# Kernel tuning notes

Measured on AMD Instinct MI355X. Metric: run time of the kernel, lower is better.

## Reference

```python
import jax, jax.numpy as jnp
import numpy as np

B, T, D, N = 4, 1024, 1024, 16
H = D // N
SCALE = H ** -0.5
NEG_INF = float('-inf')


def setup_inputs() -> dict:
    key = jax.random.key(0)
    ks = jax.random.split(key, 6)
    x = jax.random.normal(ks[0], (B, T, D), dtype=jnp.float32)
    key_padding_mask = jax.random.uniform(ks[1], (B, T)) < 0.1  # True = padded key
    # xavier-ish scaling for weights
    proj_weight = jax.random.normal(ks[2], (3 * D, D), dtype=jnp.float32) * (2.0 / (4 * D)) ** 0.5
    proj_bias = jnp.zeros((3 * D,), dtype=jnp.float32)
    sign_w = jax.random.normal(ks[3], (2 * D, D), dtype=jnp.float32) * (2.0 / (3 * D)) ** 0.5
    sign_b = jnp.zeros((2 * D,), dtype=jnp.float32)
    out_w = jax.random.normal(ks[4], (D, D), dtype=jnp.float32) * (1.0 / D) ** 0.5
    out_b = jnp.zeros((D,), dtype=jnp.float32)
    return {"x": x, "key_padding_mask": key_padding_mask,
            "proj_weight": proj_weight, "proj_bias": proj_bias,
            "sign_w": sign_w, "sign_b": sign_b,
            "out_w": out_w, "out_b": out_b}


def _heads(t):
    # [B, S, D] -> [B, N, S, H]
    return t.reshape(t.shape[0], t.shape[1], N, H).transpose(0, 2, 1, 3)


def reference(x, key_padding_mask, proj_weight, proj_bias, sign_w, sign_b, out_w, out_b):
    # self-attention path: fused in-projection, chunk order is (k, v, q)
    kvq = x @ proj_weight.T + proj_bias            # [B, T, 3D]
    k, v, q = jnp.split(kvq, 3, axis=-1)
    # sign projections (sign_q and sign_k both enabled): chunk into (sq, sk)
    sqk = x @ sign_w.T + sign_b                    # [B, T, 2D]
    sq, sk = jnp.split(sqk, 2, axis=-1)

    q, k, v = _heads(q), _heads(k), _heads(v)      # [B, N, T, H]
    sq = jax.nn.relu(_heads(sq))                   # q_activation = relu
    sk = jax.nn.relu(_heads(sk))                   # k_activation = relu

    attn_weight = jnp.einsum('bnth,bnsh->bnts', q, k) * SCALE   # [B, N, T, T]
    sign_weight = jnp.tanh(jnp.einsum('bnth,bnsh->bnts', sq, sk))

    kp = key_padding_mask[:, None, None, :]        # [B, 1, 1, T]
    attn_weight = jnp.where(kp, NEG_INF, attn_weight)
    sign_weight = jnp.where(attn_weight == NEG_INF, 0.0, sign_weight)

    ctx = jnp.einsum('bnts,bnsh->bnth', sign_weight, v)         # [B, N, T, H]
    ctx = ctx.transpose(0, 2, 1, 3).reshape(x.shape[0], x.shape[1], D)
    out = ctx @ out_w.T + out_b
    return out, sign_weight
```

## Files before the change

kernel.cpp:

```cpp
#include <hip/hip_runtime.h>

#define B_ 4
#define T_ 1024
#define D_ 1024
#define N_ 16
#define H_ 64

typedef __attribute__((ext_vector_type(8))) short bf16x8;
typedef __attribute__((ext_vector_type(4))) float f32x4;

static __device__ __forceinline__ unsigned short f2bf(float f) {
  unsigned u = __float_as_uint(f);
  u += 0x7fff + ((u >> 16) & 1);
  return (unsigned short)(u >> 16);
}

static __device__ __forceinline__ unsigned pk2(float a, float b) {
  return (unsigned)f2bf(a) | ((unsigned)f2bf(b) << 16);
}

static __device__ __forceinline__ float fast_tanh(float x) {
  float e = __expf(2.0f * x);
  return 1.0f - 2.0f / (e + 1.0f);
}

__global__ __launch_bounds__(256) void prep_kernel(
    const float* __restrict__ x, const float* __restrict__ sign_w,
    const float* __restrict__ proj_w_v, const float* __restrict__ out_w,
    const unsigned char* __restrict__ raw,
    unsigned short* __restrict__ xb, unsigned short* __restrict__ swb,
    unsigned short* __restrict__ pwb, unsigned short* __restrict__ owb,
    unsigned long long* __restrict__ mask64) {
  if (blockIdx.x == 0) {
    __shared__ int s_flag;
    if (threadIdx.x == 0) s_flag = 0;
    __syncthreads();
    int any = 0;
    for (int i = threadIdx.x; i < 4096; i += 256)
      if (i & 3) any |= (int)raw[i];
    if (any) atomicOr(&s_flag, 1);
    __syncthreads();
    int byte_mode = s_flag;
    const int* iraw = (const int*)raw;
    int w = threadIdx.x >> 6, l = threadIdx.x & 63;
    for (int k = 0; k < 16; ++k) {
      int pair = w * 16 + k;
      int idx = pair * 64 + l;
      int v = byte_mode ? (int)raw[idx] : iraw[idx];
      unsigned long long bal = __ballot(v != 0);
      if (l == 0) mask64[pair] = bal;
    }
  }
  const int n0 = 1048576, n1 = 524288, n2 = 262144;
  const int total = n0 + n1 + n2 + 262144;
  for (int i = blockIdx.x * 256 + threadIdx.x; i < total;
       i += gridDim.x * 256) {
    const float* src;
    unsigned short* dst;
    int off;
    if (i < n0) { src = x; dst = xb; off = i; }
    else if (i < n0 + n1) { src = sign_w; dst = swb; off = i - n0; }
    else if (i < n0 + n1 + n2) { src = proj_w_v; dst = pwb; off = i - n0 - n1; }
    else { src = out_w; dst = owb; off = i - n0 - n1 - n2; }
    float4 v = ((const float4*)src)[off];
    uint2 pk;
    pk.x = pk2(v.x, v.y);
    pk.y = pk2(v.z, v.w);
    ((uint2*)dst)[off] = pk;
  }
}

__global__ __launch_bounds__(256, 3) void gemm_mfma_kernel(
    const unsigned short* __restrict__ A, const unsigned short* __restrict__ W,
    const float* __restrict__ bias, void* __restrict__ Cv,
    int M, int N, int K, int relu, int out_mode) {
  __shared__ __align__(16) unsigned short As[128 * 64];
  __shared__ __align__(16) unsigned short Ws[128 * 64];
  int tid = threadIdx.x;
  int l = tid & 63, w = tid >> 6;
  int l15 = l & 15, l4 = l >> 4;
  int wr = w >> 1, wc = w & 1;
  size_t bm = (size_t)blockIdx.x * 128, bn = (size_t)blockIdx.y * 128;

  f32x4 acc[4][4];
#pragma unroll
  for (int m = 0; m < 4; ++m)
#pragma unroll
    for (int n = 0; n < 4; ++n) acc[m][n] = (f32x4){0.f, 0.f, 0.f, 0.f};

  for (int k0 = 0; k0 < K; k0 += 64) {
    __syncthreads();
#pragma unroll
    for (int i = 0; i < 4; ++i) {
      int seg = i * 256 + tid;
      int row = seg >> 3, cb = (seg & 7) << 4;
      unsigned short* lA = As + (size_t)(i * 256 + w * 64) * 8;
      unsigned short* lW = Ws + (size_t)(i * 256 + w * 64) * 8;
      __builtin_amdgcn_global_load_lds(
          (const __attribute__((address_space(1))) void*)
              ((const char*)(A + (bm + row) * K + k0) + cb),
          (__attribute__((address_space(3))) void*)lA, 16, 0, 0);
      __builtin_amdgcn_global_load_lds(
          (const __attribute__((address_space(1))) void*)
              ((const char*)(W + (bn + row) * K + k0) + cb),
          (__attribute__((address_space(3))) void*)lW, 16, 0, 0);
    }
    __syncthreads();

#pragma unroll
    for (int ks = 0; ks < 2; ++ks) {
      bf16x8 af[4], bf[4];
#pragma unroll
      for (int m = 0; m < 4; ++m)
        af[m] = *(const bf16x8*)(As + (wr * 64 + m * 16 + l15) * 64 +
                                 ks * 32 + l4 * 8);
#pragma unroll
      for (int n = 0; n < 4; ++n)
        bf[n] = *(const bf16x8*)(Ws + (wc * 64 + n * 16 + l15) * 64 +
                                 ks * 32 + l4 * 8);
#pragma unroll
      for (int m = 0; m < 4; ++m)
#pragma unroll
        for (int n = 0; n < 4; ++n)
          acc[m][n] = __builtin_amdgcn_mfma_f32_16x16x32_bf16(
              af[m], bf[n], acc[m][n], 0, 0, 0);
    }
  }

#pragma unroll
  for (int n = 0; n < 4; ++n) {
    size_t c = bn + wc * 64 + n * 16 + l15;
    float bv = bias[c];
#pragma unroll
    for (int m = 0; m < 4; ++m) {
      float o[4];
#pragma unroll
      for (int rr = 0; rr < 4; ++rr) {
        o[rr] = acc[m][n][rr] + bv;
        if (relu) o[rr] = fmaxf(o[rr], 0.0f);
      }
      size_t r0 = bm + wr * 64 + m * 16 + l4 * 4;
      if (out_mode == 0) {
        float* C = (float*)Cv;
#pragma unroll
        for (int rr = 0; rr < 4; ++rr) C[(r0 + rr) * N + c] = o[rr];
      } else if (out_mode == 1) {
        unsigned short* Cb = (unsigned short*)Cv;
#pragma unroll
        for (int rr = 0; rr < 4; ++rr) Cb[(r0 + rr) * N + c] = f2bf(o[rr]);
      } else {
        unsigned short* Cb = (unsigned short*)Cv;
        size_t bbase = (bm >> 10) << 10;
        int tloc = (int)(bm & 1023) + wr * 64 + m * 16 + l4 * 4;
        uint2 pk;
        pk.x = pk2(o[0], o[1]);
        pk.y = pk2(o[2], o[3]);
        *(uint2*)(Cb + (bbase + c) * 1024 + tloc) = pk;
      }
    }
  }
}

__global__ __launch_bounds__(256, 4) void attn_mfma_kernel(
    const unsigned short* __restrict__ sqkb,
    const unsigned short* __restrict__ vtb,
    const unsigned long long* __restrict__ mask64,
    float* __restrict__ sign_out,
    unsigned short* __restrict__ ctx) {
  __shared__ __align__(16) char sk_lds[2][64 * 128];
  __shared__ __align__(16) char vt_lds[2][64 * 128];
  __shared__ __align__(16) char p_lds[4 * 16 * 128];

  int bid = blockIdx.x;
  int tt = bid & 15;
  int bn = bid >> 4;
  int n = bn & 15, b = bn >> 4;
  int t0 = tt * 64;
  int tid = threadIdx.x;
  int l = tid & 63, w = tid >> 6;
  int l15 = l & 15, l4 = l >> 4;
  int trow_g = t0 + w * 16 + l15;

  bf16x8 aq[2];
#pragma unroll
  for (int ks = 0; ks < 2; ++ks)
    aq[ks] = *(const bf16x8*)(sqkb + (size_t)(b * 1024 + trow_g) * 2048 +
                              n * 64 + ks * 32 + l4 * 8);

  f32x4 cacc[4];
#pragma unroll
  for (int ht = 0; ht < 4; ++ht) cacc[ht] = (f32x4){0.f, 0.f, 0.f, 0.f};

  const char* sk_base = (const char*)(sqkb) + 2048 + (size_t)n * 128;
  const char* vt_base = (const char*)(vtb) + (size_t)bn * 64 * 2048;

  char* pw = p_lds + w * 2048;

#pragma unroll
  for (int i = 0; i < 2; ++i) {
    int seg = i * 256 + tid;
    int row = seg >> 3, cb = (seg & 7) << 4;
    int sc = cb ^ ((row & 7) << 4);
    __builtin_amdgcn_global_load_lds(
        (const __attribute__((address_space(1))) void*)
            (sk_base + (size_t)(b * 1024 + row) * 4096 + sc),
        (__attribute__((address_space(3))) void*)(sk_lds[0] + (i * 256 + w * 64) * 16),
        16, 0, 0);
    __builtin_amdgcn_global_load_lds(
        (const __attribute__((address_space(1))) void*)
            (vt_base + (size_t)row * 2048 + sc),
        (__attribute__((address_space(3))) void*)(vt_lds[0] + (i * 256 + w * 64) * 16),
        16, 0, 0);
  }

  int cur = 0;
  for (int ci = 0; ci < 16; ++ci) {
    int s0 = ci * 64;
    __syncthreads();

    if (ci < 15) {
      int s1 = s0 + 64;
#pragma unroll
      for (int i = 0; i < 2; ++i) {
        int seg = i * 256 + tid;
        int row = seg >> 3, cb = (seg & 7) << 4;
        int sc = cb ^ ((row & 7) << 4);
        __builtin_amdgcn_global_load_lds(
            (const __attribute__((address_space(1))) void*)
                (sk_base + (size_t)(b * 1024 + s1 + row) * 4096 + sc),
            (__attribute__((address_space(3))) void*)(sk_lds[cur ^ 1] + (i * 256 + w * 64) * 16),
            16, 0, 0);
        __builtin_amdgcn_global_load_lds(
            (const __attribute__((address_space(1))) void*)
                (vt_base + (size_t)row * 2048 + (size_t)s1 * 2 + sc),
            (__attribute__((address_space(3))) void*)(vt_lds[cur ^ 1] + (i * 256 + w * 64) * 16),
            16, 0, 0);
      }
    }

    unsigned long long mbits = mask64[b * 16 + ci];
    const char* skc = sk_lds[cur];
    const char* vtc = vt_lds[cur];

#pragma unroll
    for (int st = 0; st < 4; ++st) {
      f32x4 pc = (f32x4){0.f, 0.f, 0.f, 0.f};
      __builtin_amdgcn_s_setprio(1);
#pragma unroll
      for (int ks = 0; ks < 2; ++ks) {
        int srow = st * 16 + l15;
        bf16x8 ak = *(const bf16x8*)(skc + srow * 128 +
            ((ks * 64 + l4 * 16) ^ ((srow & 7) << 4)));
        pc = __builtin_amdgcn_mfma_f32_16x16x32_bf16(ak, aq[ks], pc, 0, 0, 0);
      }
      __builtin_amdgcn_s_setprio(0);
      f32x4 o;
#pragma unroll
      for (int rr = 0; rr < 4; ++rr) {
        int s_idx = st * 16 + l4 * 4 + rr;
        int msk = (int)((mbits >> s_idx) & 1ULL);
        o[rr] = msk ? 0.0f : fast_tanh(pc[rr]);
      }
      uint2 pk;
      pk.x = pk2(o[0], o[1]);
      pk.y = pk2(o[2], o[3]);
      *(uint2*)(pw + l15 * 128 + ((st * 32 + l4 * 8) ^ ((l15 & 7) << 4))) = pk;
    }

#pragma unroll
    for (int p = 0; p < 4; ++p) {
      int row = p * 4 + (l >> 4);
      uint2 pk = *(const uint2*)(pw + row * 128 +
                                 (((l & 15) * 8) ^ ((row & 7) << 4)));
      f32x4 o;
      o[0] = __uint_as_float(pk.x << 16);
      o[1] = __uint_as_float(pk.x & 0xffff0000u);
      o[2] = __uint_as_float(pk.y << 16);
      o[3] = __uint_as_float(pk.y & 0xffff0000u);
      __builtin_nontemporal_store(o,
          (f32x4*)(sign_out + ((size_t)bn * 1024 + t0 + w * 16 + row) * 1024 +
                   s0 + (l & 15) * 4));
    }

    __builtin_amdgcn_s_setprio(1);
#pragma unroll
    for (int ks = 0; ks < 2; ++ks) {
      bf16x8 bp = *(const bf16x8*)(pw + l15 * 128 +
          ((ks * 64 + l4 * 16) ^ ((l15 & 7) << 4)));
#pragma unroll
      for (int ht = 0; ht < 4; ++ht) {
        int hrow = ht * 16 + l15;
        bf16x8 av = *(const bf16x8*)(vtc + hrow * 128 +
            ((ks * 64 + l4 * 16) ^ ((hrow & 7) << 4)));
        cacc[ht] = __builtin_amdgcn_mfma_f32_16x16x32_bf16(
            av, bp, cacc[ht], 0, 0, 0);
      }
    }
    __builtin_amdgcn_s_setprio(0);
    cur ^= 1;
  }

#pragma unroll
  for (int ht = 0; ht < 4; ++ht) {
    uint2 pk;
    pk.x = pk2(cacc[ht][0], cacc[ht][1]);
    pk.y = pk2(cacc[ht][2], cacc[ht][3]);
    *(uint2*)(ctx + ((size_t)(b * 1024 + trow_g)) * 1024 + n * 64 + ht * 16 +
              l4 * 4) = pk;
  }
}

extern "C" void kernel_launch(void* const* d_in, const int* in_sizes, int n_in,
                              void* d_out, int out_size, void* d_ws, size_t ws_size,
                              hipStream_t stream) {
  const float* x = (const float*)d_in[0];
  const unsigned char* kp = (const unsigned char*)d_in[1];
  const float* proj_w = (const float*)d_in[2];
  const float* proj_b = (const float*)d_in[3];
  const float* sign_w = (const float*)d_in[4];
  const float* sign_b = (const float*)d_in[5];
  const float* out_w = (const float*)d_in[6];
  const float* out_b = (const float*)d_in[7];

  float* out = (float*)d_out;
  float* sign_out = out + (size_t)B_ * T_ * D_;

  char* ws = (char*)d_ws;
  unsigned short* xb   = (unsigned short*)ws;
  unsigned short* swb  = (unsigned short*)(ws + ((size_t)8 << 20));
  unsigned short* pwb  = (unsigned short*)(ws + ((size_t)12 << 20));
  unsigned short* owb  = (unsigned short*)(ws + ((size_t)14 << 20));
  unsigned short* sqkb = (unsigned short*)(ws + ((size_t)16 << 20));
  unsigned short* vtb  = (unsigned short*)(ws + ((size_t)32 << 20));
  unsigned long long* mask64 = (unsigned long long*)(ws + ((size_t)40 << 20));
  unsigned short* ctxb = xb;

  const int M = B_ * T_;

  prep_kernel<<<2048, 256, 0, stream>>>(x, sign_w, proj_w + (size_t)D_ * D_,
                                        out_w, kp, xb, swb, pwb, owb, mask64);

  {
    dim3 g(M / 128, 2048 / 128);
    gemm_mfma_kernel<<<g, 256, 0, stream>>>(xb, swb, sign_b, sqkb, M, 2048, D_, 1, 1);
  }
  {
    dim3 g(M / 128, 1024 / 128);
    gemm_mfma_kernel<<<g, 256, 0, stream>>>(xb, pwb, proj_b + D_, vtb, M, D_, D_, 0, 2);
  }
  attn_mfma_kernel<<<B_ * N_ * (T_ / 64), 256, 0, stream>>>(sqkb, vtb, mask64,
                                                            sign_out, ctxb);
  {
    dim3 g(M / 128, 1024 / 128);
    gemm_mfma_kernel<<<g, 256, 0, stream>>>(ctxb, owb, out_b, out, M, D_, D_, 0, 0);
  }
}
```

Measured before the change: 173.5 us.

## Merge sign and V projection GEMMs, shrink output GEMM tile, remap attention blocks

Merges the sign-projection GEMM and the V-projection GEMM into one launch whose grid y-index selects the weight and output mode. This removes a kernel launch and lets both fill the GPU together. The output projection now uses 64x128 tiles, giving twice as many blocks for better CU occupancy on the smaller GEMM. Attention blocks are remapped so consecutive block IDs are spread across (b,n,t) tiles, which changes which work lands on each XCD or CU, with possible effects on cache locality.

```diff
diff --git a/kernel.cpp b/kernel.cpp
--- a/kernel.cpp
+++ b/kernel.cpp
@@ -70,76 +70,79 @@
   }
 }
 
-__global__ __launch_bounds__(256, 3) void gemm_mfma_kernel(
+template <int MF, int NF>
+static __device__ __forceinline__ void gemm_core(
     const unsigned short* __restrict__ A, const unsigned short* __restrict__ W,
     const float* __restrict__ bias, void* __restrict__ Cv,
-    int M, int N, int K, int relu, int out_mode) {
-  __shared__ __align__(16) unsigned short As[128 * 64];
-  __shared__ __align__(16) unsigned short Ws[128 * 64];
-  int tid = threadIdx.x;
+    int N, int K, int relu, int out_mode, size_t bm, size_t bn,
+    unsigned short* As, unsigned short* Ws, int tid) {
   int l = tid & 63, w = tid >> 6;
   int l15 = l & 15, l4 = l >> 4;
   int wr = w >> 1, wc = w & 1;
-  size_t bm = (size_t)blockIdx.x * 128, bn = (size_t)blockIdx.y * 128;
-
-  f32x4 acc[4][4];
-#pragma unroll
-  for (int m = 0; m < 4; ++m)
-#pragma unroll
-    for (int n = 0; n < 4; ++n) acc[m][n] = (f32x4){0.f, 0.f, 0.f, 0.f};
+
+  f32x4 acc[MF][NF];
+#pragma unroll
+  for (int m = 0; m < MF; ++m)
+#pragma unroll
+    for (int n = 0; n < NF; ++n) acc[m][n] = (f32x4){0.f, 0.f, 0.f, 0.f};
 
   for (int k0 = 0; k0 < K; k0 += 64) {
     __syncthreads();
 #pragma unroll
-    for (int i = 0; i < 4; ++i) {
+    for (int i = 0; i < MF; ++i) {
       int seg = i * 256 + tid;
       int row = seg >> 3, cb = (seg & 7) << 4;
-      unsigned short* lA = As + (size_t)(i * 256 + w * 64) * 8;
-      unsigned short* lW = Ws + (size_t)(i * 256 + w * 64) * 8;
       __builtin_amdgcn_global_load_lds(
           (const __attribute__((address_space(1))) void*)
               ((const char*)(A + (bm + row) * K + k0) + cb),
-          (__attribute__((address_space(3))) void*)lA, 16, 0, 0);
+          (__attribute__((address_space(3))) void*)(As + (size_t)(i * 256 + w * 64) * 8),
+          16, 0, 0);
+    }
+#pragma unroll
+    for (int i = 0; i < NF; ++i) {
+      int seg = i * 256 + tid;
+      int row = seg >> 3, cb = (seg & 7) << 4;
       __builtin_amdgcn_global_load_lds(
           (const __attribute__((address_space(1))) void*)
               ((const char*)(W + (bn + row) * K + k0) + cb),
-          (__attribute__((address_space(3))) void*)lW, 16, 0, 0);
+          (__attribute__((address_space(3))) void*)(Ws + (size_t)(i * 256 + w * 64) * 8),
+          16, 0, 0);
     }
     __syncthreads();
 
 #pragma unroll
     for (int ks = 0; ks < 2; ++ks) {
-      bf16x8 af[4], bf[4];
-#pragma unroll
-      for (int m = 0; m < 4; ++m)
-        af[m] = *(const bf16x8*)(As + (wr * 64 + m * 16 + l15) * 64 +
+      bf16x8 af[MF], bf[NF];
+#pragma unroll
+      for (int m = 0; m < MF; ++m)
+        af[m] = *(const bf16x8*)(As + (wr * (MF * 16) + m * 16 + l15) * 64 +
                                  ks * 32 + l4 * 8);
 #pragma unroll
-      for (int n = 0; n < 4; ++n)
-        bf[n] = *(const bf16x8*)(Ws + (wc * 64 + n * 16 + l15) * 64 +
+      for (int n = 0; n < NF; ++n)
+        bf[n] = *(const bf16x8*)(Ws + (wc * (NF * 16) + n * 16 + l15) * 64 +
                                  ks * 32 + l4 * 8);
 #pragma unroll
-      for (int m = 0; m < 4; ++m)
-#pragma unroll
-        for (int n = 0; n < 4; ++n)
+      for (int m = 0; m < MF; ++m)
+#pragma unroll
+        for (int n = 0; n < NF; ++n)
           acc[m][n] = __builtin_amdgcn_mfma_f32_16x16x32_bf16(
               af[m], bf[n], acc[m][n], 0, 0, 0);
     }
   }
 
 #pragma unroll
-  for (int n = 0; n < 4; ++n) {
-    size_t c = bn + wc * 64 + n * 16 + l15;
+  for (int n = 0; n < NF; ++n) {
+    size_t c = bn + wc * (NF * 16) + n * 16 + l15;
     float bv = bias[c];
 #pragma unroll
-    for (int m = 0; m < 4; ++m) {
+    for (int m = 0; m < MF; ++m) {
       float o[4];
 #pragma unroll
       for (int rr = 0; rr < 4; ++rr) {
         o[rr] = acc[m][n][rr] + bv;
         if (relu) o[rr] = fmaxf(o[rr], 0.0f);
       }
-      size_t r0 = bm + wr * 64 + m * 16 + l4 * 4;
+      size_t r0 = bm + wr * (MF * 16) + m * 16 + l4 * 4;
       if (out_mode == 0) {
         float* C = (float*)Cv;
 #pragma unroll
@@ -151,7 +154,7 @@
       } else {
         unsigned short* Cb = (unsigned short*)Cv;
         size_t bbase = (bm >> 10) << 10;
-        int tloc = (int)(bm & 1023) + wr * 64 + m * 16 + l4 * 4;
+        int tloc = (int)(bm & 1023) + wr * (MF * 16) + m * 16 + l4 * 4;
         uint2 pk;
         pk.x = pk2(o[0], o[1]);
         pk.y = pk2(o[2], o[3]);
@@ -159,6 +162,33 @@
       }
     }
   }
+}
+
+__global__ __launch_bounds__(256, 3) void gemm_qv_kernel(
+    const unsigned short* __restrict__ xb, const unsigned short* __restrict__ swb,
+    const unsigned short* __restrict__ pwb, const float* __restrict__ sign_b,
+    const float* __restrict__ proj_b_v, unsigned short* __restrict__ sqkb,
+    unsigned short* __restrict__ vtb) {
+  __shared__ __align__(16) unsigned short As[128 * 64];
+  __shared__ __align__(16) unsigned short Ws[128 * 64];
+  size_t bm = (size_t)blockIdx.x * 128;
+  int by = blockIdx.y;
+  if (by < 16)
+    gemm_core<4, 4>(xb, swb, sign_b, sqkb, 2048, 1024, 1, 1,
+                    bm, (size_t)by * 128, As, Ws, threadIdx.x);
+  else
+    gemm_core<4, 4>(xb, pwb, proj_b_v, vtb, 1024, 1024, 0, 2,
+                    bm, (size_t)(by - 16) * 128, As, Ws, threadIdx.x);
+}
+
+__global__ __launch_bounds__(256, 3) void gemm_out_kernel(
+    const unsigned short* __restrict__ ctxb, const unsigned short* __restrict__ owb,
+    const float* __restrict__ out_b, float* __restrict__ out) {
+  __shared__ __align__(16) unsigned short As[64 * 64];
+  __shared__ __align__(16) unsigned short Ws[128 * 64];
+  gemm_core<2, 4>(ctxb, owb, out_b, out, 1024, 1024, 0, 0,
+                  (size_t)blockIdx.x * 64, (size_t)blockIdx.y * 128,
+                  As, Ws, threadIdx.x);
 }
 
 __global__ __launch_bounds__(256, 4) void attn_mfma_kernel(
@@ -171,7 +201,7 @@
   __shared__ __align__(16) char vt_lds[2][64 * 128];
   __shared__ __align__(16) char p_lds[4 * 16 * 128];
 
-  int bid = blockIdx.x;
+  int bid = (blockIdx.x & 7) * 128 + (blockIdx.x >> 3);
   int tt = bid & 15;
   int bn = bid >> 4;
   int n = bn & 15, b = bn >> 4;
@@ -341,17 +371,14 @@
                                         out_w, kp, xb, swb, pwb, owb, mask64);
 
   {
-    dim3 g(M / 128, 2048 / 128);
-    gemm_mfma_kernel<<<g, 256, 0, stream>>>(xb, swb, sign_b, sqkb, M, 2048, D_, 1, 1);
-  }
-  {
-    dim3 g(M / 128, 1024 / 128);
-    gemm_mfma_kernel<<<g, 256, 0, stream>>>(xb, pwb, proj_b + D_, vtb, M, D_, D_, 0, 2);
+    dim3 g(M / 128, 24);
+    gemm_qv_kernel<<<g, 256, 0, stream>>>(xb, swb, pwb, sign_b, proj_b + D_,
+                                          sqkb, vtb);
   }
   attn_mfma_kernel<<<B_ * N_ * (T_ / 64), 256, 0, stream>>>(sqkb, vtb, mask64,
                                                             sign_out, ctxb);
   {
-    dim3 g(M / 128, 1024 / 128);
-    gemm_mfma_kernel<<<g, 256, 0, stream>>>(ctxb, owb, out_b, out, M, D_, D_, 0, 0);
-  }
-}
+    dim3 g(M / 64, 1024 / 128);
+    gemm_out_kernel<<<g, 256, 0, stream>>>(ctxb, owb, out_b, out);
+  }
+}
```

Result: faster. 150.4 us (median of 2 runs) (-13.3%).
